# Optimization experiments

Measured on AMD Instinct MI355X. Metric: run time of the kernel, lower is better.

Reference implementation:

```python
import jax, jax.numpy as jnp
import numpy as np

B, S, D, H = 16, 1024, 768, 12
DH = D // H
DFF = 3072
EPS = 1e-5


def _layernorm(x, g, b):
    mu = jnp.mean(x, axis=-1, keepdims=True)
    var = jnp.mean(jnp.square(x - mu), axis=-1, keepdims=True)
    return (x - mu) * jax.lax.rsqrt(var + EPS) * g + b


def setup_inputs() -> dict:
    key = jax.random.key(0)
    ks = jax.random.split(key, 12)
    s = 0.02
    return {
        "x": jax.random.normal(ks[0], (B, S, D), jnp.float32),
        "ln1_g": jnp.ones((D,), jnp.float32),
        "ln1_b": jnp.zeros((D,), jnp.float32),
        "Wq": jax.random.normal(ks[1], (H, D, DH), jnp.float32) * s,
        "bq": jnp.zeros((H, DH), jnp.float32),
        "Wk": jax.random.normal(ks[2], (H, D, DH), jnp.float32) * s,
        "bk": jnp.zeros((H, DH), jnp.float32),
        "Wv": jax.random.normal(ks[3], (H, D, DH), jnp.float32) * s,
        "bv": jnp.zeros((H, DH), jnp.float32),
        "Wo": jax.random.normal(ks[4], (D, D), jnp.float32) * s,
        "bo": jnp.zeros((D,), jnp.float32),
        "ln2_g": jnp.ones((D,), jnp.float32),
        "ln2_b": jnp.zeros((D,), jnp.float32),
        "W1": jax.random.normal(ks[5], (D, DFF), jnp.float32) * s,
        "b1": jnp.zeros((DFF,), jnp.float32),
        "W2": jax.random.normal(ks[6], (DFF, D), jnp.float32) * s,
        "b2": jnp.zeros((D,), jnp.float32),
    }


def reference(x, ln1_g, ln1_b, Wq, bq, Wk, bk, Wv, bv, Wo, bo,
              ln2_g, ln2_b, W1, b1, W2, b2):
    # pre-norm MHA (all heads batched; equivalent to the per-head loop + concat)
    h = _layernorm(x, ln1_g, ln1_b)                           # [B,S,D]
    q = jnp.einsum('bsd,hdk->bhsk', h, Wq) + bq[None, :, None, :]
    k = jnp.einsum('bsd,hdk->bhsk', h, Wk) + bk[None, :, None, :]
    v = jnp.einsum('bsd,hdk->bhsk', h, Wv) + bv[None, :, None, :]
    scores = jnp.einsum('bhsk,bhtk->bhst', q, k) / jnp.sqrt(jnp.float32(DH))
    probs = jax.nn.softmax(scores, axis=-1)                   # [B,H,S,S]
    ctx = jnp.einsum('bhst,bhtk->bhsk', probs, v)             # [B,H,S,DH]
    ctx = ctx.transpose(0, 2, 1, 3).reshape(B, S, D)          # concat heads
    attn_out = ctx @ Wo + bo
    x = x + attn_out
    # pre-norm MLP (exact GELU, matching torch nn.GELU default)
    h2 = _layernorm(x, ln2_g, ln2_b)
    m = jax.nn.gelu(h2 @ W1 + b1, approximate=False) @ W2 + b2
    return x + m
```

## Files before the change

kernel.cpp:

```cpp
#include <hip/hip_runtime.h>
#include <hip/hip_bf16.h>
#include <math.h>

#define B_ 16
#define S_ 1024
#define D_ 768
#define H_ 12
#define DH_ 64
#define DFF 3072
#define M_ (B_*S_)

using short8 = __attribute__((ext_vector_type(8))) short;
using f32x4  = __attribute__((ext_vector_type(4))) float;

typedef __hip_bfloat16 bf16;

__device__ __forceinline__ bf16 f2b(float f) { return __float2bfloat16(f); }
__device__ __forceinline__ float ldf(const float* p) { return *p; }
__device__ __forceinline__ float ldf(const bf16* p) { return __bfloat162float(*p); }

__device__ __forceinline__ unsigned pkbf(float a, float b) {
  bf16 ha = f2b(a), hb = f2b(b);
  unsigned short ua = *(unsigned short*)&ha, ub = *(unsigned short*)&hb;
  return (unsigned)ua | ((unsigned)ub << 16);
}

__device__ __forceinline__ void gl2lds16(const void* g, void* l) {
  __builtin_amdgcn_global_load_lds((const __attribute__((address_space(1))) void*)g,
                                   (__attribute__((address_space(3))) void*)l, 16, 0, 0);
}

__global__ void conv_t(const float* __restrict__ in, bf16* __restrict__ out, int R, int C) {
  int tid = blockIdx.x * blockDim.x + threadIdx.x;
  if (tid >= R * C) return;
  int r = tid / C, c = tid - r * C;
  out[(size_t)c * R + r] = f2b(in[tid]);
}

__global__ void conv_wqkv(const float* __restrict__ Wq, const float* __restrict__ Wk,
                          const float* __restrict__ Wv, bf16* __restrict__ out) {
  int tid = blockIdx.x * blockDim.x + threadIdx.x;
  const int per = D_ * D_;
  if (tid >= 3 * per) return;
  const float* src = tid < per ? Wq : (tid < 2 * per ? Wk : Wv);
  int base = tid < per ? 0 : (tid < 2 * per ? D_ : 2 * D_);
  int rem = tid < per ? tid : (tid < 2 * per ? tid - per : tid - 2 * per);
  int h   = rem / (D_ * DH_);
  int rem2 = rem - h * (D_ * DH_);
  int d  = rem2 >> 6;
  int dh = rem2 & 63;
  out[(size_t)(base + h * DH_ + dh) * D_ + d] = f2b(src[rem]);
}

template <typename T>
__global__ __launch_bounds__(256) void ln_rows(const T* __restrict__ x,
                                               const float* __restrict__ g,
                                               const float* __restrict__ b,
                                               bf16* __restrict__ out, int rows) {
  int row  = blockIdx.x * 4 + (threadIdx.x >> 6);
  int lane = threadIdx.x & 63;
  if (row >= rows) return;
  const T* xr = x + (size_t)row * D_;
  float v[12];
  float sum = 0.f;
#pragma unroll
  for (int i = 0; i < 12; i++) { v[i] = ldf(xr + lane + i * 64); sum += v[i]; }
#pragma unroll
  for (int off = 32; off > 0; off >>= 1) sum += __shfl_xor(sum, off, 64);
  float mu = sum * (1.0f / 768.0f);
  float var = 0.f;
#pragma unroll
  for (int i = 0; i < 12; i++) { float d = v[i] - mu; var += d * d; }
#pragma unroll
  for (int off = 32; off > 0; off >>= 1) var += __shfl_xor(var, off, 64);
  var *= (1.0f / 768.0f);
  float rs = rsqrtf(var + 1e-5f);
  bf16* orow = out + (size_t)row * D_;
#pragma unroll
  for (int i = 0; i < 12; i++) {
    int c = lane + i * 64;
    orow[c] = f2b((v[i] - mu) * rs * g[c] + b[c]);
  }
}

#define GT 128
#define GK 32

template <int MODE>
__global__ __launch_bounds__(256) void gemm_bt(
    const bf16* __restrict__ A, const bf16* __restrict__ Bt, int K, int ldo,
    const float* __restrict__ bias0, const float* __restrict__ bias1,
    const float* __restrict__ bias2, const float* __restrict__ residf,
    const bf16* __restrict__ residb,
    float* __restrict__ outf, bf16* __restrict__ outb,
    bf16* __restrict__ qo, bf16* __restrict__ ko, bf16* __restrict__ vo) {
  __shared__ __align__(16) bf16 As[GT * GK];
  __shared__ __align__(16) bf16 Bs[GT * GK];
  const int tid  = threadIdx.x;
  const int w    = tid >> 6, lane = tid & 63;
  const int quad = lane >> 4, ln = lane & 15;
  const int lr   = lane >> 2, lc = lane & 3;

  const int id = blockIdx.y * gridDim.x + blockIdx.x;
  const int bandY = gridDim.y >> 3;
  const int xcd = id & 7, loc = id >> 3;
  const int by = xcd * bandY + (loc % bandY);
  const int bx = loc / bandY;
  const int m0 = by * GT, n0 = bx * GT;
  const int wm = (w >> 1) * 64, wn = (w & 1) * 64;

  f32x4 acc[4][4];
#pragma unroll
  for (int i = 0; i < 4; i++)
#pragma unroll
    for (int j = 0; j < 4; j++)
#pragma unroll
      for (int r = 0; r < 4; r++) acc[i][j][r] = 0.f;

  for (int k0 = 0; k0 < K; k0 += GK) {
#pragma unroll
    for (int i = 0; i < 2; i++) {
      const bf16* ga = A + (size_t)(m0 + i * 64 + w * 16 + lr) * K + k0 + lc * 8;
      gl2lds16(ga, As + (i * 64 + w * 16) * GK);
      const bf16* gb = Bt + (size_t)(n0 + i * 64 + w * 16 + lr) * K + k0 + lc * 8;
      gl2lds16(gb, Bs + (i * 64 + w * 16) * GK);
    }
    __syncthreads();
    short8 af[4], bfr[4];
#pragma unroll
    for (int t = 0; t < 4; t++) af[t]  = *(const short8*)&As[(wm + t * 16 + ln) * GK + quad * 8];
#pragma unroll
    for (int t = 0; t < 4; t++) bfr[t] = *(const short8*)&Bs[(wn + t * 16 + ln) * GK + quad * 8];
#pragma unroll
    for (int i = 0; i < 4; i++)
#pragma unroll
      for (int j = 0; j < 4; j++)
        acc[i][j] = __builtin_amdgcn_mfma_f32_16x16x32_bf16(af[i], bfr[j], acc[i][j], 0, 0, 0);
    __syncthreads();
  }

#pragma unroll
  for (int i = 0; i < 4; i++) {
#pragma unroll
    for (int j = 0; j < 4; j++) {
#pragma unroll
      for (int r = 0; r < 4; r++) {
        const int m = m0 + wm + i * 16 + quad * 4 + r;
        const int n = n0 + wn + j * 16 + ln;
        float v = acc[i][j][r];
        if (MODE == 0) {
          const int b = m >> 10, s = m & 1023;
          if (n < D_) {
            int h = n >> 6, dh = n & 63;
            qo[(((size_t)(b * H_ + h)) * S_ + s) * DH_ + dh] = f2b(v + bias0[n]);
          } else if (n < 2 * D_) {
            int nn = n - D_; int h = nn >> 6, dh = nn & 63;
            ko[(((size_t)(b * H_ + h)) * S_ + s) * DH_ + dh] = f2b(v + bias1[nn]);
          } else {
            int nn = n - 2 * D_; int h = nn >> 6, dh = nn & 63;
            vo[(((size_t)(b * H_ + h)) * DH_ + dh) * S_ + s] = f2b(v + bias2[nn]);
          }
        } else if (MODE == 1) {
          outb[(size_t)m * ldo + n] = f2b(v + bias0[n] + residf[(size_t)m * ldo + n]);
        } else if (MODE == 2) {
          float z = v + bias0[n];
          float u = 0.7978845608028654f * z * (1.0f + 0.044715f * z * z);
          float e = __expf(2.0f * u);
          float th = 1.0f - 2.0f / (e + 1.0f);
          outb[(size_t)m * ldo + n] = f2b(0.5f * z * (1.0f + th));
        } else {
          outf[(size_t)m * ldo + n] =
              v + bias0[n] + __bfloat162float(residb[(size_t)m * ldo + n]);
        }
      }
    }
  }
}

#define KSTR 72
#define VSTR 136

__global__ __launch_bounds__(256) void attn(const bf16* __restrict__ qb,
                                            const bf16* __restrict__ kb,
                                            const bf16* __restrict__ vb,
                                            bf16* __restrict__ ctx) {
  __shared__ __align__(16) bf16 Kl[128 * KSTR];
  __shared__ __align__(16) bf16 Vl[64 * VSTR];
  const int blk = blockIdx.x;
  const int qt = blk & 7, bh = blk >> 3;
  const int b = bh / H_, h = bh - b * H_;
  const bf16* q  = qb + (size_t)bh * S_ * DH_;
  const bf16* kp = kb + (size_t)bh * S_ * DH_;
  const bf16* vp = vb + (size_t)bh * DH_ * S_;
  const int tid = threadIdx.x;
  const int w = tid >> 6, lane = tid & 63;
  const int quad = lane >> 4, ln = lane & 15;
  const int qs0 = qt * 128 + w * 32;

  const int krow = tid >> 3, kc = tid & 7;
  const int vrow = tid >> 4, vc = tid & 15;

  short8 kpre[4], vpre[4];
#pragma unroll
  for (int r = 0; r < 4; r++) {
    kpre[r] = *(const short8*)&kp[(size_t)(krow + r * 32) * DH_ + kc * 8];
    vpre[r] = *(const short8*)&vp[(size_t)(vrow + r * 16) * S_ + vc * 8];
  }

  short8 qf[2][2];
#pragma unroll
  for (int qg = 0; qg < 2; qg++)
#pragma unroll
    for (int ts = 0; ts < 2; ts++)
      qf[qg][ts] = *(const short8*)&q[(size_t)(qs0 + qg * 16 + ln) * DH_ + ts * 32 + quad * 8];

  f32x4 o[2][4];
  float mi[2], li[2];
#pragma unroll
  for (int qg = 0; qg < 2; qg++) {
    mi[qg] = -3.0e38f; li[qg] = 0.f;
#pragma unroll
    for (int dt = 0; dt < 4; dt++)
#pragma unroll
      for (int r = 0; r < 4; r++) o[qg][dt][r] = 0.f;
  }

  for (int t0 = 0; t0 < S_; t0 += 128) {
    __syncthreads();
#pragma unroll
    for (int r = 0; r < 4; r++) {
      *(short8*)&Kl[(krow + r * 32) * KSTR + kc * 8] = kpre[r];
      *(short8*)&Vl[(vrow + r * 16) * VSTR + vc * 8] = vpre[r];
    }
    const int tn = (t0 + 128) & (S_ - 1);
#pragma unroll
    for (int r = 0; r < 4; r++) {
      kpre[r] = *(const short8*)&kp[(size_t)(tn + krow + r * 32) * DH_ + kc * 8];
      vpre[r] = *(const short8*)&vp[(size_t)(vrow + r * 16) * S_ + tn + vc * 8];
    }
    __syncthreads();

    f32x4 sa[2][8];
#pragma unroll
    for (int qg = 0; qg < 2; qg++)
#pragma unroll
      for (int tt = 0; tt < 8; tt++)
#pragma unroll
        for (int r = 0; r < 4; r++) sa[qg][tt][r] = 0.f;
#pragma unroll
    for (int tt = 0; tt < 8; tt++) {
      short8 ka0 = *(const short8*)&Kl[(tt * 16 + ln) * KSTR + quad * 8];
      short8 ka1 = *(const short8*)&Kl[(tt * 16 + ln) * KSTR + 32 + quad * 8];
#pragma unroll
      for (int qg = 0; qg < 2; qg++) {
        sa[qg][tt] = __builtin_amdgcn_mfma_f32_16x16x32_bf16(ka0, qf[qg][0], sa[qg][tt], 0, 0, 0);
        sa[qg][tt] = __builtin_amdgcn_mfma_f32_16x16x32_bf16(ka1, qf[qg][1], sa[qg][tt], 0, 0, 0);
      }
    }

    unsigned pk[2][8][2];
#pragma unroll
    for (int qg = 0; qg < 2; qg++) {
      float mx = -3.0e38f;
#pragma unroll
      for (int tt = 0; tt < 8; tt++)
#pragma unroll
        for (int r = 0; r < 4; r++) {
          float s = sa[qg][tt][r] * 0.125f;
          sa[qg][tt][r] = s;
          mx = fmaxf(mx, s);
        }
      mx = fmaxf(mx, __shfl_xor(mx, 16, 64));
      mx = fmaxf(mx, __shfl_xor(mx, 32, 64));
      float mnew = fmaxf(mi[qg], mx);
      float alpha = __expf(mi[qg] - mnew);
      float rs = 0.f;
#pragma unroll
      for (int tt = 0; tt < 8; tt++) {
        float p0 = __expf(sa[qg][tt][0] - mnew);
        float p1 = __expf(sa[qg][tt][1] - mnew);
        float p2 = __expf(sa[qg][tt][2] - mnew);
        float p3 = __expf(sa[qg][tt][3] - mnew);
        rs += (p0 + p1) + (p2 + p3);
        pk[qg][tt][0] = pkbf(p0, p1);
        pk[qg][tt][1] = pkbf(p2, p3);
      }
      rs += __shfl_xor(rs, 16, 64);
      rs += __shfl_xor(rs, 32, 64);
      li[qg] = li[qg] * alpha + rs;
      mi[qg] = mnew;
#pragma unroll
      for (int dt = 0; dt < 4; dt++)
#pragma unroll
        for (int r = 0; r < 4; r++) o[qg][dt][r] *= alpha;
    }

    const int src = (quad & 1) * 32 + ln;
    const bool hi = quad >= 2;
#pragma unroll
    for (int tt32 = 0; tt32 < 4; tt32++) {
#pragma unroll
      for (int qg = 0; qg < 2; qg++) {
        unsigned e0 = pk[qg][2 * tt32][0],     e1 = pk[qg][2 * tt32][1];
        unsigned o0 = pk[qg][2 * tt32 + 1][0], o1 = pk[qg][2 * tt32 + 1][1];
        unsigned a0 = __shfl((int)e0, src, 64),      b0 = __shfl((int)o0, src, 64);
        unsigned a1 = __shfl((int)e1, src, 64),      b1 = __shfl((int)o1, src, 64);
        unsigned a2 = __shfl((int)e0, src + 16, 64), b2 = __shfl((int)o0, src + 16, 64);
        unsigned a3 = __shfl((int)e1, src + 16, 64), b3 = __shfl((int)o1, src + 16, 64);
        union { unsigned u[4]; short8 s; } fr;
        fr.u[0] = hi ? b0 : a0;
        fr.u[1] = hi ? b1 : a1;
        fr.u[2] = hi ? b2 : a2;
        fr.u[3] = hi ? b3 : a3;
#pragma unroll
        for (int dt = 0; dt < 4; dt++) {
          short8 va = *(const short8*)&Vl[(dt * 16 + ln) * VSTR + tt32 * 32 + quad * 8];
          o[qg][dt] = __builtin_amdgcn_mfma_f32_16x16x32_bf16(va, fr.s, o[qg][dt], 0, 0, 0);
        }
      }
    }
  }

  __syncthreads();
  bf16* Ol = Kl;
#pragma unroll
  for (int qg = 0; qg < 2; qg++) {
    float inv = 1.0f / li[qg];
#pragma unroll
    for (int dt = 0; dt < 4; dt++)
#pragma unroll
      for (int r = 0; r < 4; r++)
        Ol[(w * 32 + qg * 16 + ln) * KSTR + dt * 16 + quad * 4 + r] = f2b(o[qg][dt][r] * inv);
  }
  __syncthreads();
  const int orow = tid >> 3, oc = tid & 7;
#pragma unroll
  for (int rd = 0; rd < 4; rd++) {
    int row = orow + rd * 32;
    short8 val = *(const short8*)&Ol[row * KSTR + oc * 8];
    *(short8*)&ctx[((size_t)(b * S_ + qt * 128 + row)) * D_ + h * DH_ + oc * 8] = val;
  }
}

extern "C" void kernel_launch(void* const* d_in, const int* in_sizes, int n_in,
                              void* d_out, int out_size, void* d_ws, size_t ws_size,
                              hipStream_t stream) {
  const float* x    = (const float*)d_in[0];
  const float* ln1g = (const float*)d_in[1];
  const float* ln1b = (const float*)d_in[2];
  const float* Wq   = (const float*)d_in[3];
  const float* bq   = (const float*)d_in[4];
  const float* Wk   = (const float*)d_in[5];
  const float* bk   = (const float*)d_in[6];
  const float* Wv   = (const float*)d_in[7];
  const float* bv   = (const float*)d_in[8];
  const float* Wo   = (const float*)d_in[9];
  const float* bo   = (const float*)d_in[10];
  const float* ln2g = (const float*)d_in[11];
  const float* ln2b = (const float*)d_in[12];
  const float* W1   = (const float*)d_in[13];
  const float* b1   = (const float*)d_in[14];
  const float* W2   = (const float*)d_in[15];
  const float* b2   = (const float*)d_in[16];

  char* ws = (char*)d_ws;
  const size_t SZ_MD = (size_t)M_ * D_ * 2;
  size_t off = 0;
  bf16* wqkvt = (bf16*)(ws + off); off += (size_t)3 * D_ * D_ * 2;
  bf16* wot   = (bf16*)(ws + off); off += (size_t)D_ * D_ * 2;
  bf16* w1t   = (bf16*)(ws + off); off += (size_t)DFF * D_ * 2;
  bf16* w2t   = (bf16*)(ws + off); off += (size_t)D_ * DFF * 2;
  bf16* h     = (bf16*)(ws + off); off += SZ_MD;
  bf16* x1    = (bf16*)(ws + off); off += SZ_MD;
  char* unionbase = ws + off;
  bf16* qbuf = (bf16*)(unionbase);
  bf16* kbuf = (bf16*)(unionbase + SZ_MD);
  bf16* vbuf = (bf16*)(unionbase + 2 * SZ_MD);
  bf16* ctx  = (bf16*)(unionbase + 3 * SZ_MD);
  bf16* a1   = (bf16*)(unionbase);

  conv_wqkv<<<(3 * D_ * D_ + 255) / 256, 256, 0, stream>>>(Wq, Wk, Wv, wqkvt);
  conv_t<<<(D_ * D_ + 255) / 256, 256, 0, stream>>>(Wo, wot, D_, D_);
  conv_t<<<(D_ * DFF + 255) / 256, 256, 0, stream>>>(W1, w1t, D_, DFF);
  conv_t<<<(D_ * DFF + 255) / 256, 256, 0, stream>>>(W2, w2t, DFF, D_);
  ln_rows<float><<<M_ / 4, 256, 0, stream>>>(x, ln1g, ln1b, h, M_);

  gemm_bt<0><<<dim3(3 * D_ / GT, M_ / GT), 256, 0, stream>>>(
      h, wqkvt, D_, 0, bq, bk, bv, nullptr, nullptr, nullptr, nullptr,
      qbuf, kbuf, vbuf);

  attn<<<B_ * H_ * (S_ / 128), 256, 0, stream>>>(qbuf, kbuf, vbuf, ctx);

  gemm_bt<1><<<dim3(D_ / GT, M_ / GT), 256, 0, stream>>>(
      ctx, wot, D_, D_, bo, nullptr, nullptr, x, nullptr, nullptr, x1,
      nullptr, nullptr, nullptr);

  ln_rows<bf16><<<M_ / 4, 256, 0, stream>>>(x1, ln2g, ln2b, h, M_);
  gemm_bt<2><<<dim3(DFF / GT, M_ / GT), 256, 0, stream>>>(
      h, w1t, D_, DFF, b1, nullptr, nullptr, nullptr, nullptr, nullptr, a1,
      nullptr, nullptr, nullptr);

  gemm_bt<3><<<dim3(D_ / GT, M_ / GT), 256, 0, stream>>>(
      a1, w2t, DFF, D_, b2, nullptr, nullptr, nullptr, x1, (float*)d_out,
      nullptr, nullptr, nullptr, nullptr);
}
```

Before: 784.9 us.

## Double-buffer LDS tiles in bf16 GEMM to overlap global loads with MFMA

```diff
diff --git a/kernel.cpp b/kernel.cpp
--- a/kernel.cpp
+++ b/kernel.cpp
@@ -94,12 +94,12 @@
     const bf16* __restrict__ residb,
     float* __restrict__ outf, bf16* __restrict__ outb,
     bf16* __restrict__ qo, bf16* __restrict__ ko, bf16* __restrict__ vo) {
-  __shared__ __align__(16) bf16 As[GT * GK];
-  __shared__ __align__(16) bf16 Bs[GT * GK];
+  __shared__ __align__(16) bf16 As[2][GT * GK];
+  __shared__ __align__(16) bf16 Bs[2][GT * GK];
   const int tid  = threadIdx.x;
   const int w    = tid >> 6, lane = tid & 63;
   const int quad = lane >> 4, ln = lane & 15;
-  const int lr   = lane >> 2, lc = lane & 3;
+  const int lr   = lane >> 2, lc = (lane & 3) * 8;
 
   const int id = blockIdx.y * gridDim.x + blockIdx.x;
   const int bandY = gridDim.y >> 3;
@@ -117,20 +117,37 @@
 #pragma unroll
       for (int r = 0; r < 4; r++) acc[i][j][r] = 0.f;
 
-  for (int k0 = 0; k0 < K; k0 += GK) {
-#pragma unroll
-    for (int i = 0; i < 2; i++) {
-      const bf16* ga = A + (size_t)(m0 + i * 64 + w * 16 + lr) * K + k0 + lc * 8;
-      gl2lds16(ga, As + (i * 64 + w * 16) * GK);
-      const bf16* gb = Bt + (size_t)(n0 + i * 64 + w * 16 + lr) * K + k0 + lc * 8;
-      gl2lds16(gb, Bs + (i * 64 + w * 16) * GK);
-    }
-    __syncthreads();
+  const int T = K / GK;
+
+  const bf16* gA0 = A  + (size_t)(m0 + w * 16 + lr) * K + lc;
+  const bf16* gA1 = A  + (size_t)(m0 + 64 + w * 16 + lr) * K + lc;
+  const bf16* gB0 = Bt + (size_t)(n0 + w * 16 + lr) * K + lc;
+  const bf16* gB1 = Bt + (size_t)(n0 + 64 + w * 16 + lr) * K + lc;
+
+  gl2lds16(gA0, &As[0][(w * 16) * GK]);
+  gl2lds16(gA1, &As[0][(64 + w * 16) * GK]);
+  gl2lds16(gB0, &Bs[0][(w * 16) * GK]);
+  gl2lds16(gB1, &Bs[0][(64 + w * 16) * GK]);
+  __syncthreads();
+
+#pragma unroll 2
+  for (int t = 0; t < T; t++) {
+    if (t + 1 < T) {
+      const int kk = (t + 1) * GK;
+      bf16* An = As[(t + 1) & 1];
+      bf16* Bn = Bs[(t + 1) & 1];
+      gl2lds16(gA0 + kk, &An[(w * 16) * GK]);
+      gl2lds16(gA1 + kk, &An[(64 + w * 16) * GK]);
+      gl2lds16(gB0 + kk, &Bn[(w * 16) * GK]);
+      gl2lds16(gB1 + kk, &Bn[(64 + w * 16) * GK]);
+    }
+    const bf16* Asc = As[t & 1];
+    const bf16* Bsc = Bs[t & 1];
     short8 af[4], bfr[4];
 #pragma unroll
-    for (int t = 0; t < 4; t++) af[t]  = *(const short8*)&As[(wm + t * 16 + ln) * GK + quad * 8];
-#pragma unroll
-    for (int t = 0; t < 4; t++) bfr[t] = *(const short8*)&Bs[(wn + t * 16 + ln) * GK + quad * 8];
+    for (int u = 0; u < 4; u++) af[u]  = *(const short8*)&Asc[(wm + u * 16 + ln) * GK + quad * 8];
+#pragma unroll
+    for (int u = 0; u < 4; u++) bfr[u] = *(const short8*)&Bsc[(wn + u * 16 + ln) * GK + quad * 8];
 #pragma unroll
     for (int i = 0; i < 4; i++)
 #pragma unroll
```

Result: faster. 751.0 us (-4.3%).
